# Performance work log

Hardware: AMD Instinct MI355X
Metric: run time of the kernel (lower is better)

Reference implementation:

```python
import jax, jax.numpy as jnp
import numpy as np
from jax import lax

N, T, U, V = 32, 512, 100, 4096
BLANK = 0


def setup_inputs() -> dict:
    key = jax.random.key(0)
    k1, k2, k3, k4, k5 = jax.random.split(key, 5)
    encoder_out = jax.random.normal(k1, (N, T, V), dtype=jnp.float32)
    decoder_out = jax.random.normal(k2, (N, U + 1, V), dtype=jnp.float32)
    targets = jax.random.randint(k3, (N, U), 1, V)            # labels, never blank
    input_lengths = jax.random.randint(k4, (N,), T // 2, T + 1)
    target_lengths = jax.random.randint(k5, (N,), U // 2, U + 1)
    return {
        "encoder_out": encoder_out,
        "decoder_out": decoder_out,
        "targets": targets,
        "input_lengths": input_lengths,
        "target_lengths": target_lengths,
    }


def _logprob_single(enc, dec, y, in_len, tgt_len):
    # enc: (T, V)  dec: (U+1, V)  y: (U,)
    Um = y.shape[0]
    u_idx = jnp.arange(Um)
    # emit[t, u] = enc[t, y[u]] + dec[u, y[u]]  (cost of emitting label u+1 at time t)
    emit = enc[:, y] + dec[u_idx, y][None, :]          # (T, U)
    blank_e = enc[:, BLANK]                            # (T,)
    blank_d = dec[:, BLANK]                            # (U+1,)

    # t = 0 row: alpha[0, u] = sum_{k<u} emit[0, k]
    alpha0 = jnp.concatenate([jnp.zeros((1,), enc.dtype), jnp.cumsum(emit[0])])

    def row_step(alpha_prev, xs):
        be_prev, emit_t = xs
        # blank transition from row t-1 (same u)
        top = alpha_prev + be_prev + blank_d           # (U+1,)

        # label transition within row: alpha[u] = logaddexp(top[u], alpha[u-1] + emit_t[u-1])
        def u_step(carry, x):
            top_u, em = x
            a = jnp.logaddexp(top_u, carry + em)
            return a, a

        _, rest = lax.scan(u_step, top[0], (top[1:], emit_t))
        alpha = jnp.concatenate([top[:1], rest])
        return alpha, alpha

    _, rows = lax.scan(row_step, alpha0, (blank_e[:-1], emit[1:]))
    alphas = jnp.concatenate([alpha0[None, :], rows], axis=0)   # (T, U+1)

    # log p(y|x) = alpha[T-1, U] + enc[T-1, blank] + dec[U, blank] with true lengths
    return alphas[in_len - 1, tgt_len] + enc[in_len - 1, BLANK] + dec[tgt_len, BLANK]


def reference(encoder_out, decoder_out, targets, input_lengths, target_lengths):
    # reduction='none': returns per-utterance log p(y|x), shape (N,)
    return jax.vmap(_logprob_single)(encoder_out, decoder_out, targets,
                                     input_lengths, target_lengths)
```

## Files before the change

### kernel.cpp

```cpp
#include <hip/hip_runtime.h>

#define NB 32
#define TT 512
#define UU 100
#define UM 101
#define VV 4096
#define NEG (-1e30f)
#define PD 16
#define DMAX 672
#define L2E 1.4426950408889634f
#define LN2 0.6931471805599453f

__device__ __forceinline__ float vexp2(float x){ float r; asm("v_exp_f32 %0, %1" : "=v"(r) : "v"(x)); return r; }
__device__ __forceinline__ float vlog2(float x){ float r; asm("v_log_f32 %0, %1" : "=v"(r) : "v"(x)); return r; }

__device__ __forceinline__ float lae2(float a, float b) {
    float m  = fmaxf(a, b);
    float nd = -fabsf(a - b);
    return m + vlog2(1.0f + vexp2(nd));
}

__global__ void prep_k(const float* __restrict__ enc, const float* __restrict__ dec,
                       const int* __restrict__ tgt,
                       float* __restrict__ blk, float* __restrict__ bdv,
                       float* __restrict__ dvx) {
    int n = blockIdx.x, tid = threadIdx.x;
    blk[n * TT + tid] = enc[((size_t)n * TT + tid) * VV] * L2E;
    if (tid < UM) bdv[n * UM + tid] = dec[((size_t)n * UM + tid) * VV] * L2E;
    if (tid < UU) {
        int y = tgt[n * UU + tid];
        dvx[n * UU + tid] = dec[((size_t)n * UM + tid) * VV + y] * L2E;
    }
}

__global__ void build_k(const float* __restrict__ enc, const int* __restrict__ tgt,
                        const int* __restrict__ ilen, const int* __restrict__ tlen,
                        const float* __restrict__ blk, const float* __restrict__ bdv,
                        const float* __restrict__ dvx, float4* __restrict__ st) {
    int n = blockIdx.y;
    int d = blockIdx.x * 4 + (threadIdx.x >> 6);
    int lane = threadIdx.x & 63;
    int tin = ilen[n], tg = tlen[n];
    const float* encn = enc + (size_t)n * TT * VV;
    float4 v;
    {
        int u = 2 * lane, t = d - u;
        float e = NEG, b = NEG;
        if (u >= 1 && u <= tg && t >= 0 && t < tin)
            e = fmaf(encn[(size_t)t * VV + tgt[n * UU + u - 1]], L2E, dvx[n * UU + u - 1]);
        if (u <= UU && t >= 1 && t < TT)
            b = blk[n * TT + t - 1] + bdv[n * UM + u];
        v.x = e; v.y = b;
    }
    {
        int u = 2 * lane + 1, t = d - u;
        float e = NEG, b = NEG;
        if (u <= tg && t >= 0 && t < tin)
            e = fmaf(encn[(size_t)t * VV + tgt[n * UU + u - 1]], L2E, dvx[n * UU + u - 1]);
        if (u <= UU && t >= 1 && t < TT)
            b = blk[n * TT + t - 1] + bdv[n * UM + u];
        v.z = e; v.w = b;
    }
    st[((size_t)n * DMAX + d) * 64 + lane] = v;
}

__global__ __launch_bounds__(64) void dp_k(const int* __restrict__ ilen,
                                           const int* __restrict__ tlen,
                                           const float4* __restrict__ st,
                                           const float* __restrict__ blk,
                                           const float* __restrict__ bdv,
                                           float* __restrict__ out) {
    int n = blockIdx.x;
    int lane = threadIdx.x;
    int tin = ilen[n], tg = tlen[n];
    int dend = tin - 1 + tg;
    const float4* sp = st + ((size_t)n * DMAX) * 64 + lane;
    bool cap0 = (2 * lane == tg), cap1 = (2 * lane + 1 == tg);
    bool fx16 = (lane == 16), fx32 = (lane == 32), fx48 = (lane == 48);

    float a0 = (lane == 0) ? 0.0f : NEG;
    float a1 = NEG;
    float res = NEG;

    auto STEP = [&](float4 v, int dd) {
        int sh = __builtin_amdgcn_update_dpp(__float_as_int(NEG), __float_as_int(a1),
                                             0x111, 0xF, 0xF, false);
        float s15 = __int_as_float(__builtin_amdgcn_readlane(__float_as_int(a1), 15));
        float s31 = __int_as_float(__builtin_amdgcn_readlane(__float_as_int(a1), 31));
        float s47 = __int_as_float(__builtin_amdgcn_readlane(__float_as_int(a1), 47));
        float l0 = __int_as_float(sh);
        l0 = fx16 ? s15 : l0;
        l0 = fx32 ? s31 : l0;
        l0 = fx48 ? s47 : l0;
        float bt0 = a0 + v.y, et0 = l0 + v.x;
        float bt1 = a1 + v.w, et1 = a0 + v.z;
        a0 = lae2(bt0, et0);
        a1 = lae2(bt1, et1);
        if (dd == dend) { if (cap0) res = a0; if (cap1) res = a1; }
    };

    float4 A[PD], B[PD];
#pragma unroll
    for (int k = 0; k < PD; ++k) A[k] = sp[(size_t)(1 + k) * 64];
    __builtin_amdgcn_sched_barrier(0);

    for (int d = 1; d <= dend; d += 2 * PD) {
#pragma unroll
        for (int k = 0; k < PD; ++k) B[k] = sp[(size_t)(d + PD + k) * 64];
        __builtin_amdgcn_sched_barrier(0);
#pragma unroll
        for (int k = 0; k < PD; ++k) STEP(A[k], d + k);
        __builtin_amdgcn_sched_barrier(0);
#pragma unroll
        for (int k = 0; k < PD; ++k) A[k] = sp[(size_t)(d + 2 * PD + k) * 64];
        __builtin_amdgcn_sched_barrier(0);
#pragma unroll
        for (int k = 0; k < PD; ++k) STEP(B[k], d + PD + k);
        __builtin_amdgcn_sched_barrier(0);
    }

    float fin  = blk[n * TT + (tin - 1)];
    float bdtg = bdv[n * UM + tg];
    if (cap0 | cap1) out[n] = (res + fin + bdtg) * LN2;
}

extern "C" void kernel_launch(void* const* d_in, const int* in_sizes, int n_in,
                              void* d_out, int out_size, void* d_ws, size_t ws_size,
                              hipStream_t hs) {
    const float* enc  = (const float*)d_in[0];
    const float* dec  = (const float*)d_in[1];
    const int*   tgt  = (const int*)d_in[2];
    const int*   ilen = (const int*)d_in[3];
    const int*   tlen = (const int*)d_in[4];
    float* out = (float*)d_out;

    float4* st  = (float4*)d_ws;
    float*  blk = (float*)(st + (size_t)NB * DMAX * 64);
    float*  bdv = blk + NB * TT;
    float*  dvx = bdv + NB * UM;

    hipLaunchKernelGGL(prep_k,  dim3(NB), dim3(512), 0, hs, enc, dec, tgt, blk, bdv, dvx);
    hipLaunchKernelGGL(build_k, dim3(DMAX / 4, NB), dim3(256), 0, hs,
                       enc, tgt, ilen, tlen, blk, bdv, dvx, st);
    hipLaunchKernelGGL(dp_k,    dim3(NB), dim3(64), 0, hs, ilen, tlen, st, blk, bdv, out);
}
```

Measured before the change: 83.01 us.

## Shrink staged DP stream to emit-only float2, build blank terms from LDS

The build kernel now writes only the two emit terms per lane (float2 instead of float4), which halves the global staging traffic. The DP kernel rebuilds the blank-transition terms on the fly from an LDS copy of the per-frame blank scores plus per-lane decoder blank values held in registers. The bdv array is padded to 128 entries per utterance. Prefetch depth goes from 16 to 24, and lae2 computes min-max instead of -|a-b|. This adds LDS reads and register pressure in the serial DP loop in exchange for less global memory bandwidth.

```diff
diff --git a/kernel.cpp b/kernel.cpp
--- a/kernel.cpp
+++ b/kernel.cpp
@@ -6,7 +6,7 @@
 #define UM 101
 #define VV 4096
 #define NEG (-1e30f)
-#define PD 16
+#define PD 24
 #define DMAX 672
 #define L2E 1.4426950408889634f
 #define LN2 0.6931471805599453f
@@ -16,7 +16,7 @@
 
 __device__ __forceinline__ float lae2(float a, float b) {
     float m  = fmaxf(a, b);
-    float nd = -fabsf(a - b);
+    float nd = fminf(a, b) - m;
     return m + vlog2(1.0f + vexp2(nd));
 }
 
@@ -26,7 +26,8 @@
                        float* __restrict__ dvx) {
     int n = blockIdx.x, tid = threadIdx.x;
     blk[n * TT + tid] = enc[((size_t)n * TT + tid) * VV] * L2E;
-    if (tid < UM) bdv[n * UM + tid] = dec[((size_t)n * UM + tid) * VV] * L2E;
+    if (tid < 128)
+        bdv[n * 128 + tid] = (tid < UM) ? dec[((size_t)n * UM + tid) * VV] * L2E : 0.0f;
     if (tid < UU) {
         int y = tgt[n * UU + tid];
         dvx[n * UU + tid] = dec[((size_t)n * UM + tid) * VV + y] * L2E;
@@ -35,46 +36,47 @@
 
 __global__ void build_k(const float* __restrict__ enc, const int* __restrict__ tgt,
                         const int* __restrict__ ilen, const int* __restrict__ tlen,
-                        const float* __restrict__ blk, const float* __restrict__ bdv,
-                        const float* __restrict__ dvx, float4* __restrict__ st) {
+                        const float* __restrict__ dvx, float2* __restrict__ st) {
     int n = blockIdx.y;
     int d = blockIdx.x * 4 + (threadIdx.x >> 6);
     int lane = threadIdx.x & 63;
     int tin = ilen[n], tg = tlen[n];
     const float* encn = enc + (size_t)n * TT * VV;
-    float4 v;
+    float e0 = NEG, e1 = NEG;
     {
         int u = 2 * lane, t = d - u;
-        float e = NEG, b = NEG;
         if (u >= 1 && u <= tg && t >= 0 && t < tin)
-            e = fmaf(encn[(size_t)t * VV + tgt[n * UU + u - 1]], L2E, dvx[n * UU + u - 1]);
-        if (u <= UU && t >= 1 && t < TT)
-            b = blk[n * TT + t - 1] + bdv[n * UM + u];
-        v.x = e; v.y = b;
+            e0 = fmaf(encn[(size_t)t * VV + tgt[n * UU + u - 1]], L2E, dvx[n * UU + u - 1]);
     }
     {
         int u = 2 * lane + 1, t = d - u;
-        float e = NEG, b = NEG;
         if (u <= tg && t >= 0 && t < tin)
-            e = fmaf(encn[(size_t)t * VV + tgt[n * UU + u - 1]], L2E, dvx[n * UU + u - 1]);
-        if (u <= UU && t >= 1 && t < TT)
-            b = blk[n * TT + t - 1] + bdv[n * UM + u];
-        v.z = e; v.w = b;
+            e1 = fmaf(encn[(size_t)t * VV + tgt[n * UU + u - 1]], L2E, dvx[n * UU + u - 1]);
     }
-    st[((size_t)n * DMAX + d) * 64 + lane] = v;
+    st[((size_t)n * DMAX + d) * 64 + lane] = make_float2(e0, e1);
 }
 
-__global__ __launch_bounds__(64) void dp_k(const int* __restrict__ ilen,
-                                           const int* __restrict__ tlen,
-                                           const float4* __restrict__ st,
-                                           const float* __restrict__ blk,
-                                           const float* __restrict__ bdv,
-                                           float* __restrict__ out) {
+__global__ __launch_bounds__(64, 1) void dp_k(const int* __restrict__ ilen,
+                                              const int* __restrict__ tlen,
+                                              const float2* __restrict__ st,
+                                              const float* __restrict__ blk,
+                                              const float* __restrict__ bdv,
+                                              float* __restrict__ out) {
     int n = blockIdx.x;
     int lane = threadIdx.x;
     int tin = ilen[n], tg = tlen[n];
     int dend = tin - 1 + tg;
-    const float4* sp = st + ((size_t)n * DMAX) * 64 + lane;
+
+    __shared__ float blkL[864];
+    for (int i = lane; i < 864; i += 64) blkL[i] = NEG;
+    __syncthreads();
+    for (int t = lane; t < TT; t += 64) blkL[128 + t] = blk[n * TT + t];
+    __syncthreads();
+
+    float bd0 = bdv[n * 128 + 2 * lane];
+    float bd1 = bdv[n * 128 + 2 * lane + 1];
+    const float2* sp = st + ((size_t)n * DMAX) * 64 + lane;
+    int ib = 126 - 2 * lane;
     bool cap0 = (2 * lane == tg), cap1 = (2 * lane + 1 == tg);
     bool fx16 = (lane == 16), fx32 = (lane == 32), fx48 = (lane == 48);
 
@@ -82,7 +84,20 @@
     float a1 = NEG;
     float res = NEG;
 
-    auto STEP = [&](float4 v, int dd) {
+    float Ae0[PD], Ae1[PD], Ab0[PD], Ab1[PD];
+    float Be0[PD], Be1[PD], Bb0[PD], Bb1[PD];
+
+#define LOADR(E0, E1, B0, B1, K, DD)                                   \
+    {                                                                   \
+        int dc = min((DD), DMAX - 1);                                   \
+        float2 ev = sp[(size_t)dc * 64];                                \
+        float b1s = blkL[ib + dc];                                      \
+        float b0s = blkL[ib + dc + 1];                                  \
+        E0[K] = ev.x; E1[K] = ev.y;                                     \
+        B0[K] = b0s + bd0; B1[K] = b1s + bd1;                           \
+    }
+
+    auto STEP = [&](float e0, float e1, float bb0, float bb1, int dd) {
         int sh = __builtin_amdgcn_update_dpp(__float_as_int(NEG), __float_as_int(a1),
                                              0x111, 0xF, 0xF, false);
         float s15 = __int_as_float(__builtin_amdgcn_readlane(__float_as_int(a1), 15));
@@ -92,36 +107,36 @@
         l0 = fx16 ? s15 : l0;
         l0 = fx32 ? s31 : l0;
         l0 = fx48 ? s47 : l0;
-        float bt0 = a0 + v.y, et0 = l0 + v.x;
-        float bt1 = a1 + v.w, et1 = a0 + v.z;
+        float bt0 = a0 + bb0, et0 = l0 + e0;
+        float bt1 = a1 + bb1, et1 = a0 + e1;
         a0 = lae2(bt0, et0);
         a1 = lae2(bt1, et1);
         if (dd == dend) { if (cap0) res = a0; if (cap1) res = a1; }
     };
 
-    float4 A[PD], B[PD];
 #pragma unroll
-    for (int k = 0; k < PD; ++k) A[k] = sp[(size_t)(1 + k) * 64];
+    for (int k = 0; k < PD; ++k) LOADR(Ae0, Ae1, Ab0, Ab1, k, 1 + k);
     __builtin_amdgcn_sched_barrier(0);
 
     for (int d = 1; d <= dend; d += 2 * PD) {
 #pragma unroll
-        for (int k = 0; k < PD; ++k) B[k] = sp[(size_t)(d + PD + k) * 64];
+        for (int k = 0; k < PD; ++k) LOADR(Be0, Be1, Bb0, Bb1, k, d + PD + k);
         __builtin_amdgcn_sched_barrier(0);
 #pragma unroll
-        for (int k = 0; k < PD; ++k) STEP(A[k], d + k);
+        for (int k = 0; k < PD; ++k) STEP(Ae0[k], Ae1[k], Ab0[k], Ab1[k], d + k);
         __builtin_amdgcn_sched_barrier(0);
 #pragma unroll
-        for (int k = 0; k < PD; ++k) A[k] = sp[(size_t)(d + 2 * PD + k) * 64];
+        for (int k = 0; k < PD; ++k) LOADR(Ae0, Ae1, Ab0, Ab1, k, d + 2 * PD + k);
         __builtin_amdgcn_sched_barrier(0);
 #pragma unroll
-        for (int k = 0; k < PD; ++k) STEP(B[k], d + PD + k);
+        for (int k = 0; k < PD; ++k) STEP(Be0[k], Be1[k], Bb0[k], Bb1[k], d + PD + k);
         __builtin_amdgcn_sched_barrier(0);
     }
 
-    float fin  = blk[n * TT + (tin - 1)];
-    float bdtg = bdv[n * UM + tg];
+    float fin  = blkL[128 + tin - 1];
+    float bdtg = bdv[n * 128 + tg];
     if (cap0 | cap1) out[n] = (res + fin + bdtg) * LN2;
+#undef LOADR
 }
 
 extern "C" void kernel_launch(void* const* d_in, const int* in_sizes, int n_in,
@@ -134,13 +149,13 @@
     const int*   tlen = (const int*)d_in[4];
     float* out = (float*)d_out;
 
-    float4* st  = (float4*)d_ws;
+    float2* st  = (float2*)d_ws;
     float*  blk = (float*)(st + (size_t)NB * DMAX * 64);
     float*  bdv = blk + NB * TT;
-    float*  dvx = bdv + NB * UM;
+    float*  dvx = bdv + NB * 128;
 
     hipLaunchKernelGGL(prep_k,  dim3(NB), dim3(512), 0, hs, enc, dec, tgt, blk, bdv, dvx);
     hipLaunchKernelGGL(build_k, dim3(DMAX / 4, NB), dim3(256), 0, hs,
-                       enc, tgt, ilen, tlen, blk, bdv, dvx, st);
+                       enc, tgt, ilen, tlen, dvx, st);
     hipLaunchKernelGGL(dp_k,    dim3(NB), dim3(64), 0, hs, ilen, tlen, st, blk, bdv, out);
 }
```

Result: slower. 87.45 us (+5.3%).
